# Kernel tuning notes

Measured on AMD Instinct MI355X. Metric: run time of the kernel, lower is better.

## Reference

```python
import jax, jax.numpy as jnp
import numpy as np
import math

# model dims
B, S, T = 4, 256, 8
D_MODEL, D_STATE, N_HEAD, NUM_LAYERS = 256, 128, 4, 2
VOCAB = 32000
D_HEAD = D_STATE // N_HEAD
# AdaptiveLIFNeuron constants
TAU, BASE_THR, ADAPT, TARGET = 2.0, 1.0, 0.1, 0.02
DECAY = math.exp(-1.0 / TAU)


@jax.custom_vjp
def spike_fn(x):
    # spikingjelly surrogate.ATan forward = heaviside
    return (x >= 0).astype(x.dtype)

def _spike_fwd(x):
    return spike_fn(x), x

def _spike_bwd(x, g):
    # ATan surrogate gradient, alpha=2: 1 / (1 + (pi*x)^2)
    return (g / (1.0 + (math.pi * x) ** 2),)

spike_fn.defvjp(_spike_fwd, _spike_bwd)


def lif_step(x, v, thr):
    v_pot = v * DECAY + x
    spike = spike_fn(v_pot - jax.lax.stop_gradient(thr))
    v_new = v_pot * (1.0 - jax.lax.stop_gradient(spike))  # reset where spiked
    err = jax.lax.stop_gradient(spike.mean() - TARGET)    # torch.no_grad threshold update
    thr_new = jnp.maximum(thr + ADAPT * err, 0.5)
    return spike, v_new, thr_new


def ssm_layer(x_tbsd, A, C, Wq, bq, Wkv, bkv, Wo, bo):
    # x_tbsd: [T, B, S, d_model] spikes/embeddings, scanned over time
    scale = 1.0 / math.sqrt(D_HEAD)

    def step(carry, x_t):
        h, sv, ov, ts, to = carry
        st = h @ A.T                                      # [B,S,d_state]
        q = (h @ Wq.T + bq).reshape(B * S, N_HEAD, D_HEAD)
        kv = x_t @ Wkv.T + bkv                            # [B,S,2*d_state]
        k, v = jnp.split(kv, 2, axis=-1)
        k = k.reshape(B * S, N_HEAD, D_HEAD)
        v = v.reshape(B * S, N_HEAD, D_HEAD)
        # attention across all B*S positions (faithful to torch reshape)
        scores = jnp.einsum('ahd,bhd->hab', q, k) * scale  # [H, BS, BS]
        attn = jax.nn.softmax(scores, axis=-1)
        att = jnp.einsum('hab,bhd->ahd', attn, v).reshape(B, S, D_STATE)
        upd = st + att @ Wo.T + bo
        h2, sv2, ts2 = lif_step(upd, sv, ts)
        out_pot = h2 @ C.T                                 # [B,S,d_model]
        os_, ov2, to2 = lif_step(out_pot, ov, to)
        return (h2, sv2, ov2, ts2, to2), os_

    init = (jnp.zeros((B, S, D_STATE)), jnp.zeros((B, S, D_STATE)),
            jnp.zeros((B, S, D_MODEL)),
            jnp.full((D_STATE,), BASE_THR), jnp.full((D_MODEL,), BASE_THR))
    _, outs = jax.lax.scan(step, init, x_tbsd)
    return outs  # [T,B,S,d_model]


def setup_inputs() -> dict:
    key = jax.random.key(0)
    ks = jax.random.split(key, 8)
    nrm = lambda k, shape, s: jax.random.normal(k, shape, jnp.float32) * s
    L = NUM_LAYERS
    return {
        'input_ids': jax.random.randint(ks[0], (B, S), 0, VOCAB),
        'emb': nrm(ks[1], (VOCAB, D_MODEL), 0.02),
        'A': nrm(ks[2], (L, D_STATE, D_STATE), 1.0 / math.sqrt(D_STATE)),
        'C': nrm(ks[3], (L, D_MODEL, D_STATE), 1.0 / math.sqrt(D_STATE)),
        'Wq': nrm(ks[4], (L, D_STATE, D_STATE), 1.0 / math.sqrt(D_STATE)),
        'bq': jnp.zeros((L, D_STATE)),
        'Wkv': nrm(ks[5], (L, 2 * D_STATE, D_MODEL), 1.0 / math.sqrt(D_MODEL)),
        'bkv': jnp.zeros((L, 2 * D_STATE)),
        'Wo': nrm(ks[6], (L, D_STATE, D_STATE), 1.0 / math.sqrt(D_STATE)),
        'bo': jnp.zeros((L, D_STATE)),
        'Wout': nrm(ks[7], (VOCAB, D_MODEL), 1.0 / math.sqrt(D_MODEL)),
        'bout': jnp.zeros((VOCAB,)),
    }


def reference(input_ids, emb, A, C, Wq, bq, Wkv, bkv, Wo, bo, Wout, bout):
    tok = emb[input_ids]                                   # [B,S,d_model]
    # encoder_type='expand': replicate embedding over time steps
    hidden = jnp.broadcast_to(tok[None], (T, B, S, D_MODEL))
    for l in range(NUM_LAYERS):
        hidden = ssm_layer(hidden, A[l], C[l], Wq[l], bq[l],
                           Wkv[l], bkv[l], Wo[l], bo[l])
    time_integrated = hidden.mean(axis=0)                  # mean over time -> [B,S,d_model]
    logits = time_integrated @ Wout.T + bout               # output_projection -> [B,S,vocab]
    return logits
```

## Files before the change

### kernel.cpp

```cpp
#include <hip/hip_runtime.h>
#include <math.h>

#define BS_TOT   1024
#define DM       256
#define DST      128
#define TSTEPS   8
#define DECAYF   0.6065306597126334f
#define SCALEF   0.17677669529663689f
#define NE       (BS_TOT * DM)

__global__ void embed_k(const int* __restrict__ ids, const float* __restrict__ emb,
                        float* __restrict__ tok) {
    int r = blockIdx.x, c = threadIdx.x;
    tok[r * DM + c] = emb[(size_t)ids[r] * DM + c];
}

__global__ void init_k(float* __restrict__ hb0, float* __restrict__ hb1,
                       float* __restrict__ svb0, float* __restrict__ svb1,
                       float* __restrict__ ovb0, float* __restrict__ ovb1,
                       int* __restrict__ cnts) {
    int i = blockIdx.x * 256 + threadIdx.x;
    if (i < BS_TOT * DST) { hb0[i] = 0.f; hb1[i] = 0.f; svb0[i] = 0.f; svb1[i] = 0.f; }
    ovb0[i] = 0.f; ovb1[i] = 0.f;
    if (i < 16) cnts[i] = 0;
}

__global__ __launch_bounds__(256) void ktrans_k(const float* __restrict__ kv,
                                                float* __restrict__ kT) {
    __shared__ float tile[64][133];
    const float* src = kv + (size_t)blockIdx.y * NE;
    float* dst = kT + (size_t)blockIdx.y * (128 * 1024);
    const int kc = blockIdx.x, tid = threadIdx.x;
#pragma unroll
    for (int i = 0; i < 32; ++i) {
        int idx = i * 256 + tid;
        int key = idx >> 7, d = idx & 127;
        tile[key][d] = src[(size_t)(kc * 64 + key) * 256 + d];
    }
    __syncthreads();
#pragma unroll
    for (int i = 0; i < 32; ++i) {
        int idx = i * 256 + tid;
        int d = idx >> 6, key = idx & 63;
        dst[(size_t)d * 1024 + kc * 64 + key] = tile[key][d];
    }
}

__global__ void mean_k(const float* __restrict__ outs, float* __restrict__ ti) {
    int i = blockIdx.x * 256 + threadIdx.x;
    float s = 0.f;
#pragma unroll
    for (int t = 0; t < TSTEPS; ++t) s += outs[t * NE + i];
    ti[i] = s * 0.125f;
}

template <int BM, int BN, int BK, int TM, int TN>
__global__ __launch_bounds__((BM / TM) * (BN / TN))
void gemm_k(const float* __restrict__ Amat, const float* __restrict__ Wmat,
            const float* __restrict__ bias, float* __restrict__ outp,
            int M, int N, int K) {
    constexpr int NT  = (BM / TM) * (BN / TN);
    constexpr int NXT = BN / TN;
    __shared__ float As[BK][BM + 4];
    __shared__ float Bs[BK][BN + 4];
    const int tid = threadIdx.x;
    const int n0 = blockIdx.x * BN, m0 = blockIdx.y * BM;
    const int tx = tid % NXT, ty = tid / NXT;
    float acc[TM][TN] = {};

    for (int k0 = 0; k0 < K; k0 += BK) {
#pragma unroll
        for (int i = 0; i < (BM * BK) / NT; ++i) {
            int idx = i * NT + tid;
            int kk = idx % BK, mm = idx / BK;
            As[kk][mm] = Amat[(size_t)(m0 + mm) * K + k0 + kk];
        }
#pragma unroll
        for (int i = 0; i < (BN * BK) / NT; ++i) {
            int idx = i * NT + tid;
            int kk = idx % BK, nn = idx / BK;
            Bs[kk][nn] = Wmat[(size_t)(n0 + nn) * K + k0 + kk];
        }
        __syncthreads();
#pragma unroll
        for (int kk = 0; kk < BK; ++kk) {
            float a[TM], b[TN];
#pragma unroll
            for (int i = 0; i < TM; ++i) a[i] = As[kk][ty * TM + i];
#pragma unroll
            for (int j = 0; j < TN; ++j) b[j] = Bs[kk][tx * TN + j];
#pragma unroll
            for (int i = 0; i < TM; ++i)
#pragma unroll
                for (int j = 0; j < TN; ++j) acc[i][j] += a[i] * b[j];
        }
        __syncthreads();
    }
#pragma unroll
    for (int i = 0; i < TM; ++i) {
        int mr = m0 + ty * TM + i;
#pragma unroll
        for (int j = 0; j < TN; ++j) {
            int nc = n0 + tx * TN + j;
            float x = acc[i][j];
            if (bias) x += bias[nc];
            outp[(size_t)mr * N + nc] = x;
        }
    }
}

__global__ __launch_bounds__(256) void fstep_k(
    const float* __restrict__ kT,
    const float* __restrict__ kv,
    const float* __restrict__ A_w,
    const float* __restrict__ Wq_w,
    const float* __restrict__ bq_w,
    const float* __restrict__ Wo_w,
    const float* __restrict__ bo_w,
    const float* __restrict__ C_w,
    const float* __restrict__ h_old, float* __restrict__ h_new,
    const float* __restrict__ sv_in, float* __restrict__ sv_out,
    const float* __restrict__ ov_in, float* __restrict__ ov_out,
    const float* __restrict__ att_in, float* __restrict__ att_out,
    float* __restrict__ outs_prev,
    int* __restrict__ cnt1, int* __restrict__ cnt2, int t, int do_B)
{
    __shared__ float p_s[8][1032];
    __shared__ float v_s[2][64 * 36];
    __shared__ float hA_s[8 * 128];
    __shared__ float h2_s[8 * 128];
    __shared__ float att_s[8 * 128];
    __shared__ float q_s[8 * 36];
    __shared__ float red_s[8 * 33];
    __shared__ float mrow_s[8], linv_s[8], thr_s[2];

    const int tid = threadIdx.x;
    const int hh = blockIdx.x >> 7;
    const int r0 = (blockIdx.x & 127) * 8;
    const bool wrb = (hh == 0);

    if (t > 0) {
        if (tid == 0) {
            float ts = 1.0f, to = 1.0f;
            for (int i = 0; i < t - 1; ++i) {
                float e1 = (float)cnt1[i] * (1.f / 131072.f) - 0.02f;
                ts = fmaxf(ts + 0.1f * e1, 0.5f);
                float e2 = (float)cnt2[i] * (1.f / 262144.f) - 0.02f;
                to = fmaxf(to + 0.1f * e2, 0.5f);
            }
            thr_s[0] = ts; thr_s[1] = to;
        }
#pragma unroll
        for (int i = 0; i < 4; ++i) {
            int idx = i * 256 + tid;
            hA_s[idx]  = h_old[r0 * 128 + idx];
            att_s[idx] = att_in[r0 * 128 + idx];
        }
        __syncthreads();

        {
            const int n = tid & 127, half = tid >> 7;
            const float* Ar  = A_w  + n * 128;
            const float* Wor = Wo_w + n * 128;
            float st[4] = {0.f, 0.f, 0.f, 0.f};
            float b[4]  = {0.f, 0.f, 0.f, 0.f};
            for (int k4 = 0; k4 < 32; ++k4) {
                const int k = k4 * 4;
                float4 wa = *(const float4*)(Ar + k);
                float4 wo = *(const float4*)(Wor + k);
#pragma unroll
                for (int r4 = 0; r4 < 4; ++r4) {
                    int r = half * 4 + r4;
                    float4 hv = *(const float4*)&hA_s[r * 128 + k];
                    float4 av = *(const float4*)&att_s[r * 128 + k];
                    st[r4] += hv.x * wa.x; st[r4] += hv.y * wa.y;
                    st[r4] += hv.z * wa.z; st[r4] += hv.w * wa.w;
                    b[r4] += av.x * wo.x; b[r4] += av.y * wo.y;
                    b[r4] += av.z * wo.z; b[r4] += av.w * wo.w;
                }
            }
            float ts = thr_s[0];
            int my1 = 0;
#pragma unroll
            for (int r4 = 0; r4 < 4; ++r4) {
                int r = half * 4 + r4, row = r0 + r;
                float x = b[r4] + bo_w[n];
                x += st[r4];
                float v = sv_in[row * 128 + n];
                float vp = v * DECAYF + x;
                float sp = (vp - ts >= 0.f) ? 1.f : 0.f;
                h2_s[r * 128 + n] = sp;
                if (wrb) {
                    h_new[row * 128 + n]  = sp;
                    sv_out[row * 128 + n] = vp * (1.f - sp);
                }
                my1 += (int)sp;
            }
            if (wrb) {
#pragma unroll
                for (int off = 32; off > 0; off >>= 1) my1 += __shfl_down(my1, off, 64);
                if ((tid & 63) == 0) atomicAdd(&cnt1[t - 1], my1);
            }
        }
        __syncthreads();

        if (wrb) {
            const int n = tid;
            const float* Cr = C_w + n * 128;
            float acc[8] = {0.f, 0.f, 0.f, 0.f, 0.f, 0.f, 0.f, 0.f};
            for (int k4 = 0; k4 < 32; ++k4) {
                const int k = k4 * 4;
                float4 wc = *(const float4*)(Cr + k);
#pragma unroll
                for (int r = 0; r < 8; ++r) {
                    float4 hv = *(const float4*)&h2_s[r * 128 + k];
                    acc[r] += hv.x * wc.x; acc[r] += hv.y * wc.y;
                    acc[r] += hv.z * wc.z; acc[r] += hv.w * wc.w;
                }
            }
            float to = thr_s[1];
            int my2 = 0;
#pragma unroll
            for (int r = 0; r < 8; ++r) {
                int row = r0 + r;
                float vo = ov_in[row * 256 + n];
                float vp = vo * DECAYF + acc[r];
                float sp = (vp - to >= 0.f) ? 1.f : 0.f;
                outs_prev[(size_t)row * 256 + n] = sp;
                ov_out[row * 256 + n] = vp * (1.f - sp);
                my2 += (int)sp;
            }
#pragma unroll
            for (int off = 32; off > 0; off >>= 1) my2 += __shfl_down(my2, off, 64);
            if ((tid & 63) == 0) atomicAdd(&cnt2[t - 1], my2);
        }
    } else {
#pragma unroll
        for (int i = 0; i < 4; ++i) {
            int idx = i * 256 + tid;
            h2_s[idx] = h_new[r0 * 128 + idx];
        }
        __syncthreads();
    }

    if (!do_B) return;

    {
        const int r = tid >> 5, d = tid & 31;
        const int j = hh * 32 + d;
        const float* Wqr = Wq_w + j * 128;
        float acc = 0.f;
        for (int k4 = 0; k4 < 32; ++k4) {
            const int k = k4 * 4;
            float4 wv = *(const float4*)(Wqr + k);
            float4 hv = *(const float4*)&h2_s[r * 128 + k];
            acc += hv.x * wv.x; acc += hv.y * wv.y;
            acc += hv.z * wv.z; acc += hv.w * wv.w;
        }
        q_s[r * 36 + d] = acc + bq_w[j];
    }
    __syncthreads();

    {
        const int w = tid >> 6, lane = tid & 63;
        float4 qr0[8], qr1[8];
#pragma unroll
        for (int d4 = 0; d4 < 8; ++d4) {
            qr0[d4] = *(const float4*)&q_s[(2 * w) * 36 + d4 * 4];
            qr1[d4] = *(const float4*)&q_s[(2 * w + 1) * 36 + d4 * 4];
        }
        const float* kTh = kT + hh * 32 * 1024;
        for (int kk = 0; kk < 16; ++kk) {
            const int key = kk * 64 + lane;
            float kreg[32];
#pragma unroll
            for (int d = 0; d < 32; ++d) kreg[d] = kTh[d * 1024 + key];
            float a0 = 0.f, a1 = 0.f;
#pragma unroll
            for (int d4 = 0; d4 < 8; ++d4) {
                a0 += qr0[d4].x * kreg[d4 * 4 + 0]; a0 += qr0[d4].y * kreg[d4 * 4 + 1];
                a0 += qr0[d4].z * kreg[d4 * 4 + 2]; a0 += qr0[d4].w * kreg[d4 * 4 + 3];
                a1 += qr1[d4].x * kreg[d4 * 4 + 0]; a1 += qr1[d4].y * kreg[d4 * 4 + 1];
                a1 += qr1[d4].z * kreg[d4 * 4 + 2]; a1 += qr1[d4].w * kreg[d4 * 4 + 3];
            }
            p_s[2 * w][key]     = a0 * SCALEF;
            p_s[2 * w + 1][key] = a1 * SCALEF;
        }
    }
    __syncthreads();

    {
        const int rh = tid >> 5, lg = tid & 31;
        float mx = -1e30f;
        for (int jj = 0; jj < 32; ++jj) mx = fmaxf(mx, p_s[rh][lg + 32 * jj]);
        red_s[rh * 33 + lg] = mx;
        __syncthreads();
        if (tid < 8) {
            float m = red_s[tid * 33];
            for (int j = 1; j < 32; ++j) m = fmaxf(m, red_s[tid * 33 + j]);
            mrow_s[tid] = m;
        }
        __syncthreads();
        float m = mrow_s[rh];
        float ls = 0.f;
        for (int jj = 0; jj < 32; ++jj) {
            int a = lg + 32 * jj;
            float p = expf(p_s[rh][a] - m);
            p_s[rh][a] = p;
            ls += p;
        }
        red_s[rh * 33 + lg] = ls;
        __syncthreads();
        if (tid < 8) {
            float l = 0.f;
            for (int j = 0; j < 32; ++j) l += red_s[tid * 33 + j];
            linv_s[tid] = 1.0f / l;
        }
    }
    __syncthreads();

    {
        const int rp = (tid >> 4) & 3;
        const int dp = tid & 15;
        const float4* kv4 = (const float4*)kv;
        float4 stg0, stg1;
        {
            int i0 = tid, i1 = 256 + tid;
            stg0 = kv4[(size_t)(i0 >> 3) * 64 + 32 + hh * 8 + (i0 & 7)];
            stg1 = kv4[(size_t)(i1 >> 3) * 64 + 32 + hh * 8 + (i1 & 7)];
        }
        float a00 = 0.f, a01 = 0.f, a10 = 0.f, a11 = 0.f;
        for (int c = 0; c < 16; ++c) {
            float* vb = &v_s[c & 1][0];
            {
                int i0 = tid, i1 = 256 + tid;
                *(float4*)&vb[(i0 >> 3) * 36 + (i0 & 7) * 4] = stg0;
                *(float4*)&vb[(i1 >> 3) * 36 + (i1 & 7) * 4] = stg1;
            }
            if (c < 15) {
                int i0 = tid, i1 = 256 + tid;
                stg0 = kv4[(size_t)((c + 1) * 64 + (i0 >> 3)) * 64 + 32 + hh * 8 + (i0 & 7)];
                stg1 = kv4[(size_t)((c + 1) * 64 + (i1 >> 3)) * 64 + 32 + hh * 8 + (i1 & 7)];
            }
            __syncthreads();
            if (tid < 64) {
#pragma unroll 4
                for (int k4 = 0; k4 < 16; ++k4) {
                    const int kb = k4 * 4;
                    float4 p0 = *(const float4*)&p_s[2 * rp][c * 64 + kb];
                    float4 p1 = *(const float4*)&p_s[2 * rp + 1][c * 64 + kb];
                    float2 v0 = *(const float2*)&vb[(kb + 0) * 36 + 2 * dp];
                    float2 v1 = *(const float2*)&vb[(kb + 1) * 36 + 2 * dp];
                    float2 v2 = *(const float2*)&vb[(kb + 2) * 36 + 2 * dp];
                    float2 v3 = *(const float2*)&vb[(kb + 3) * 36 + 2 * dp];
                    a00 += p0.x * v0.x; a01 += p0.x * v0.y;
                    a10 += p1.x * v0.x; a11 += p1.x * v0.y;
                    a00 += p0.y * v1.x; a01 += p0.y * v1.y;
                    a10 += p1.y * v1.x; a11 += p1.y * v1.y;
                    a00 += p0.z * v2.x; a01 += p0.z * v2.y;
                    a10 += p1.z * v2.x; a11 += p1.z * v2.y;
                    a00 += p0.w * v3.x; a01 += p0.w * v3.y;
                    a10 += p1.w * v3.x; a11 += p1.w * v3.y;
                }
            }
        }
        if (tid < 64) {
            float li0 = linv_s[2 * rp], li1 = linv_s[2 * rp + 1];
            *(float2*)&att_out[(size_t)(r0 + 2 * rp) * 128 + hh * 32 + 2 * dp] =
                make_float2(a00 * li0, a01 * li0);
            *(float2*)&att_out[(size_t)(r0 + 2 * rp + 1) * 128 + hh * 32 + 2 * dp] =
                make_float2(a10 * li1, a11 * li1);
        }
    }
}

extern "C" void kernel_launch(void* const* d_in, const int* in_sizes, int n_in,
                              void* d_out, int out_size, void* d_ws, size_t ws_size,
                              hipStream_t stream) {
    (void)in_sizes; (void)n_in; (void)out_size; (void)ws_size;
    const int*   ids  = (const int*)d_in[0];
    const float* emb  = (const float*)d_in[1];
    const float* Aw   = (const float*)d_in[2];
    const float* Cw   = (const float*)d_in[3];
    const float* Wq   = (const float*)d_in[4];
    const float* bq   = (const float*)d_in[5];
    const float* Wkv  = (const float*)d_in[6];
    const float* bkv  = (const float*)d_in[7];
    const float* Wo   = (const float*)d_in[8];
    const float* bo   = (const float*)d_in[9];
    const float* Wout = (const float*)d_in[10];
    const float* bout = (const float*)d_in[11];
    float* out = (float*)d_out;
    float* ws  = (float*)d_ws;

    float* tok  = ws;
    float* bufA = tok  + NE;
    float* bufB = bufA + 8 * NE;
    float* kvb  = bufB + 8 * NE;
    float* kTb  = kvb  + 8 * NE;
    float* attb0 = kTb  + 8 * 131072;
    float* attb1 = attb0 + 131072;
    float* hb0  = attb1 + 131072;
    float* hb1  = hb0  + 131072;
    float* svb0 = hb1  + 131072;
    float* svb1 = svb0 + 131072;
    float* ovb0 = svb1 + 131072;
    float* ovb1 = ovb0 + 262144;
    float* ti   = ovb1 + 262144;
    int*   cnts = (int*)(ti + NE);

    float* hb[2]   = {hb0, hb1};
    float* svb[2]  = {svb0, svb1};
    float* ovb[2]  = {ovb0, ovb1};
    float* attb[2] = {attb0, attb1};

    embed_k<<<dim3(1024), dim3(256), 0, stream>>>(ids, emb, tok);

    for (int l = 0; l < 2; ++l) {
        const float* Al   = Aw  + l * 16384;
        const float* Cl   = Cw  + l * 32768;
        const float* Wql  = Wq  + l * 16384;
        const float* bql  = bq  + l * 128;
        const float* Wkvl = Wkv + l * 65536;
        const float* bkvl = bkv + l * 256;
        const float* Wol  = Wo  + l * 16384;
        const float* bol  = bo  + l * 128;
        const float* xin  = (l == 0) ? tok : bufA;
        float* outs       = (l == 0) ? bufA : bufB;
        const int Mkv     = (l == 0) ? BS_TOT : 8 * BS_TOT;
        const int nt      = (l == 0) ? 1 : 8;

        init_k<<<dim3(1024), dim3(256), 0, stream>>>(hb0, hb1, svb0, svb1,
                                                     ovb0, ovb1, cnts);

        gemm_k<64, 64, 16, 4, 4><<<dim3(256 / 64, Mkv / 64), dim3(256), 0, stream>>>(
            xin, Wkvl, bkvl, kvb, Mkv, 256, 256);

        ktrans_k<<<dim3(16, nt), dim3(256), 0, stream>>>(kvb, kTb);

        for (int t = 0; t <= TSTEPS; ++t) {
            const int do_B = (t < TSTEPS) ? 1 : 0;
            const int tt = (t < TSTEPS) ? t : (TSTEPS - 1);
            const float* kT_t = (l == 0) ? kTb : kTb + (size_t)tt * 131072;
            const float* kv_t = (l == 0) ? kvb : kvb + (size_t)tt * NE;
            float* outs_prev = outs + (size_t)((t > 0) ? (t - 1) : 0) * NE;
            const int grid = do_B ? 512 : 128;
            fstep_k<<<dim3(grid), dim3(256), 0, stream>>>(
                kT_t, kv_t, Al, Wql, bql, Wol, bol, Cl,
                hb[t & 1], hb[(t + 1) & 1],
                svb[t & 1], svb[(t + 1) & 1],
                ovb[t & 1], ovb[(t + 1) & 1],
                attb[(t + 1) & 1], attb[t & 1],
                outs_prev, cnts, cnts + 8, t, do_B);
        }
    }

    mean_k<<<dim3(1024), dim3(256), 0, stream>>>(bufB, ti);

    gemm_k<64, 64, 16, 4, 4><<<dim3(32000 / 64, BS_TOT / 64), dim3(256), 0, stream>>>(
        ti, Wout, bout, out, BS_TOT, 32000, 256);
}
```

Before: 1.351 ms.

## Split fused step kernel into LIF and attention kernels with spike-sparse matvecs

```diff
diff --git a/kernel.cpp b/kernel.cpp
--- a/kernel.cpp
+++ b/kernel.cpp
@@ -15,13 +15,23 @@
     tok[r * DM + c] = emb[(size_t)ids[r] * DM + c];
 }
 
-__global__ void init_k(float* __restrict__ hb0, float* __restrict__ hb1,
-                       float* __restrict__ svb0, float* __restrict__ svb1,
-                       float* __restrict__ ovb0, float* __restrict__ ovb1,
+__global__ void prep_k(float* __restrict__ h, float* __restrict__ sv, float* __restrict__ ov,
+                       float* __restrict__ W1T, float* __restrict__ WoT, float* __restrict__ CT,
+                       const float* __restrict__ Al, const float* __restrict__ Wql,
+                       const float* __restrict__ Wol, const float* __restrict__ Cl,
                        int* __restrict__ cnts) {
     int i = blockIdx.x * 256 + threadIdx.x;
-    if (i < BS_TOT * DST) { hb0[i] = 0.f; hb1[i] = 0.f; svb0[i] = 0.f; svb1[i] = 0.f; }
-    ovb0[i] = 0.f; ovb1[i] = 0.f;
+    if (i < BS_TOT * DST) { h[i] = 0.f; sv[i] = 0.f; }
+    ov[i] = 0.f;
+    if (i < 32768) {
+        int k = i >> 8, n = i & 255;
+        W1T[i] = (n < 128) ? Al[n * 128 + k] : Wql[(n - 128) * 128 + k];
+        CT[i]  = Cl[n * 128 + k];
+    }
+    if (i < 16384) {
+        int k = i >> 7, n = i & 127;
+        WoT[i] = Wol[n * 128 + k];
+    }
     if (i < 16) cnts[i] = 0;
 }
 
@@ -109,182 +119,250 @@
     }
 }
 
-__global__ __launch_bounds__(256) void fstep_k(
+__global__ __launch_bounds__(256) void lif_k(
+    const float* __restrict__ W1T,
+    const float* __restrict__ WoT,
+    const float* __restrict__ CT,
+    const float* __restrict__ bq_w,
+    const float* __restrict__ bo_w,
+    float* __restrict__ h,
+    float* __restrict__ sv,
+    float* __restrict__ ov,
+    const float* __restrict__ att_in,
+    float* __restrict__ outs_prev,
+    float* __restrict__ q_g,
+    int* __restrict__ cnt1, int* __restrict__ cnt2, int t, int do_B)
+{
+    __shared__ float hA_s[4 * 128];
+    __shared__ float h2_s[4 * 128];
+    __shared__ float att_s[4 * 128];
+    __shared__ unsigned long long umr_s[4][2];
+    __shared__ unsigned long long um_s[2];
+    __shared__ float thr_s[2];
+
+    const int tid = threadIdx.x;
+    const int r0 = blockIdx.x * 4;
+
+    if (tid == 0) {
+        float ts = 1.0f, to = 1.0f;
+        for (int i = 0; i < t - 1; ++i) {
+            float e1 = (float)cnt1[i] * (1.f / 131072.f) - 0.02f;
+            ts = fmaxf(ts + 0.1f * e1, 0.5f);
+            float e2 = (float)cnt2[i] * (1.f / 262144.f) - 0.02f;
+            to = fmaxf(to + 0.1f * e2, 0.5f);
+        }
+        thr_s[0] = ts; thr_s[1] = to;
+    }
+    hA_s[tid]       = h[r0 * 128 + tid];
+    hA_s[256 + tid] = h[r0 * 128 + 256 + tid];
+    if (t > 0) {
+        att_s[tid]       = att_in[r0 * 128 + tid];
+        att_s[256 + tid] = att_in[r0 * 128 + 256 + tid];
+    }
+    __syncthreads();
+    {
+        int w = tid >> 6, l = tid & 63;
+        unsigned long long b0 = __ballot(hA_s[w * 128 + l] != 0.f);
+        unsigned long long b1 = __ballot(hA_s[w * 128 + 64 + l] != 0.f);
+        if (l == 0) { umr_s[w][0] = b0; umr_s[w][1] = b1; }
+    }
+    __syncthreads();
+    if (tid == 0) {
+        um_s[0] = umr_s[0][0] | umr_s[1][0] | umr_s[2][0] | umr_s[3][0];
+        um_s[1] = umr_s[0][1] | umr_s[1][1] | umr_s[2][1] | umr_s[3][1];
+    }
+    __syncthreads();
+
+    const int n = tid & 127, half = tid >> 7;
+    const int ra = half * 2, rb = half * 2 + 1;
+
+    if (t > 0) {
+        float sta = 0.f, stb = 0.f;
+        unsigned long long u = um_s[0];
+        while (u) {
+            int k = __builtin_ctzll(u); u &= u - 1;
+            float w = W1T[(k << 8) + n];
+            sta += hA_s[ra * 128 + k] * w; stb += hA_s[rb * 128 + k] * w;
+        }
+        u = um_s[1];
+        while (u) {
+            int kk = __builtin_ctzll(u); u &= u - 1;
+            int k = 64 + kk;
+            float w = W1T[(k << 8) + n];
+            sta += hA_s[ra * 128 + k] * w; stb += hA_s[rb * 128 + k] * w;
+        }
+        float ba = 0.f, bb = 0.f;
+        for (int i4 = 0; i4 < 32; ++i4) {
+            const int i = i4 * 4;
+            float w0 = WoT[(i + 0) * 128 + n];
+            float w1 = WoT[(i + 1) * 128 + n];
+            float w2 = WoT[(i + 2) * 128 + n];
+            float w3 = WoT[(i + 3) * 128 + n];
+            float4 aa = *(const float4*)&att_s[ra * 128 + i];
+            float4 ab = *(const float4*)&att_s[rb * 128 + i];
+            ba += aa.x * w0; ba += aa.y * w1; ba += aa.z * w2; ba += aa.w * w3;
+            bb += ab.x * w0; bb += ab.y * w1; bb += ab.z * w2; bb += ab.w * w3;
+        }
+        float ts = thr_s[0];
+        float xa = ba + bo_w[n]; xa += sta;
+        float va = sv[(r0 + ra) * 128 + n];
+        float vpa = va * DECAYF + xa;
+        float spa = (vpa - ts >= 0.f) ? 1.f : 0.f;
+        h[(r0 + ra) * 128 + n]  = spa;
+        sv[(r0 + ra) * 128 + n] = vpa * (1.f - spa);
+        h2_s[ra * 128 + n] = spa;
+
+        float xb = bb + bo_w[n]; xb += stb;
+        float vb = sv[(r0 + rb) * 128 + n];
+        float vpb = vb * DECAYF + xb;
+        float spb = (vpb - ts >= 0.f) ? 1.f : 0.f;
+        h[(r0 + rb) * 128 + n]  = spb;
+        sv[(r0 + rb) * 128 + n] = vpb * (1.f - spb);
+        h2_s[rb * 128 + n] = spb;
+
+        unsigned long long bba = __ballot(spa != 0.f);
+        unsigned long long bbb = __ballot(spb != 0.f);
+        int w = tid >> 6, l = tid & 63;
+        if (l == 0) {
+            umr_s[ra][w & 1] = bba;
+            umr_s[rb][w & 1] = bbb;
+            atomicAdd(&cnt1[t - 1], __popcll(bba) + __popcll(bbb));
+        }
+    } else {
+        h2_s[tid]       = hA_s[tid];
+        h2_s[256 + tid] = hA_s[256 + tid];
+    }
+    __syncthreads();
+    if (tid == 0) {
+        um_s[0] = umr_s[0][0] | umr_s[1][0] | umr_s[2][0] | umr_s[3][0];
+        um_s[1] = umr_s[0][1] | umr_s[1][1] | umr_s[2][1] | umr_s[3][1];
+    }
+    __syncthreads();
+
+    if (t > 0) {
+        const int n2 = tid;
+        float a0 = 0.f, a1 = 0.f, a2 = 0.f, a3 = 0.f;
+        unsigned long long u = um_s[0];
+        while (u) {
+            int k = __builtin_ctzll(u); u &= u - 1;
+            float w = CT[(k << 8) + n2];
+            a0 += h2_s[k] * w;       a1 += h2_s[128 + k] * w;
+            a2 += h2_s[256 + k] * w; a3 += h2_s[384 + k] * w;
+        }
+        u = um_s[1];
+        while (u) {
+            int kk = __builtin_ctzll(u); u &= u - 1;
+            int k = 64 + kk;
+            float w = CT[(k << 8) + n2];
+            a0 += h2_s[k] * w;       a1 += h2_s[128 + k] * w;
+            a2 += h2_s[256 + k] * w; a3 += h2_s[384 + k] * w;
+        }
+        float to = thr_s[1];
+        float accs[4] = {a0, a1, a2, a3};
+        float sp[4];
+#pragma unroll
+        for (int r = 0; r < 4; ++r) {
+            float vo = ov[(r0 + r) * 256 + n2];
+            float vp = vo * DECAYF + accs[r];
+            float s = (vp - to >= 0.f) ? 1.f : 0.f;
+            sp[r] = s;
+            outs_prev[(size_t)(r0 + r) * 256 + n2] = s;
+            ov[(r0 + r) * 256 + n2] = vp * (1.f - s);
+        }
+        unsigned long long c0 = __ballot(sp[0] != 0.f);
+        unsigned long long c1 = __ballot(sp[1] != 0.f);
+        unsigned long long c2 = __ballot(sp[2] != 0.f);
+        unsigned long long c3 = __ballot(sp[3] != 0.f);
+        if ((tid & 63) == 0)
+            atomicAdd(&cnt2[t - 1], __popcll(c0) + __popcll(c1) + __popcll(c2) + __popcll(c3));
+    }
+
+    if (do_B) {
+        float qa = 0.f, qb = 0.f;
+        unsigned long long u = um_s[0];
+        while (u) {
+            int k = __builtin_ctzll(u); u &= u - 1;
+            float w = W1T[(k << 8) + 128 + n];
+            qa += h2_s[ra * 128 + k] * w; qb += h2_s[rb * 128 + k] * w;
+        }
+        u = um_s[1];
+        while (u) {
+            int kk = __builtin_ctzll(u); u &= u - 1;
+            int k = 64 + kk;
+            float w = W1T[(k << 8) + 128 + n];
+            qa += h2_s[ra * 128 + k] * w; qb += h2_s[rb * 128 + k] * w;
+        }
+        q_g[(r0 + ra) * 128 + n] = qa + bq_w[n];
+        q_g[(r0 + rb) * 128 + n] = qb + bq_w[n];
+    }
+}
+
+__global__ __launch_bounds__(256) void attn_k(
+    const float* __restrict__ q_g,
     const float* __restrict__ kT,
     const float* __restrict__ kv,
-    const float* __restrict__ A_w,
-    const float* __restrict__ Wq_w,
-    const float* __restrict__ bq_w,
-    const float* __restrict__ Wo_w,
-    const float* __restrict__ bo_w,
-    const float* __restrict__ C_w,
-    const float* __restrict__ h_old, float* __restrict__ h_new,
-    const float* __restrict__ sv_in, float* __restrict__ sv_out,
-    const float* __restrict__ ov_in, float* __restrict__ ov_out,
-    const float* __restrict__ att_in, float* __restrict__ att_out,
-    float* __restrict__ outs_prev,
-    int* __restrict__ cnt1, int* __restrict__ cnt2, int t, int do_B)
+    float* __restrict__ att_out)
 {
     __shared__ float p_s[8][1032];
-    __shared__ float v_s[2][64 * 36];
-    __shared__ float hA_s[8 * 128];
-    __shared__ float h2_s[8 * 128];
-    __shared__ float att_s[8 * 128];
-    __shared__ float q_s[8 * 36];
+    __shared__ float v_s[64 * 36];
+    __shared__ float q_s[8][32];
     __shared__ float red_s[8 * 33];
-    __shared__ float mrow_s[8], linv_s[8], thr_s[2];
+    __shared__ float mrow_s[8], linv_s[8];
 
     const int tid = threadIdx.x;
     const int hh = blockIdx.x >> 7;
     const int r0 = (blockIdx.x & 127) * 8;
-    const bool wrb = (hh == 0);
-
-    if (t > 0) {
-        if (tid == 0) {
-            float ts = 1.0f, to = 1.0f;
-            for (int i = 0; i < t - 1; ++i) {
-                float e1 = (float)cnt1[i] * (1.f / 131072.f) - 0.02f;
-                ts = fmaxf(ts + 0.1f * e1, 0.5f);
-                float e2 = (float)cnt2[i] * (1.f / 262144.f) - 0.02f;
-                to = fmaxf(to + 0.1f * e2, 0.5f);
-            }
-            thr_s[0] = ts; thr_s[1] = to;
-        }
-#pragma unroll
-        for (int i = 0; i < 4; ++i) {
-            int idx = i * 256 + tid;
-            hA_s[idx]  = h_old[r0 * 128 + idx];
-            att_s[idx] = att_in[r0 * 128 + idx];
-        }
-        __syncthreads();
-
-        {
-            const int n = tid & 127, half = tid >> 7;
-            const float* Ar  = A_w  + n * 128;
-            const float* Wor = Wo_w + n * 128;
-            float st[4] = {0.f, 0.f, 0.f, 0.f};
-            float b[4]  = {0.f, 0.f, 0.f, 0.f};
-            for (int k4 = 0; k4 < 32; ++k4) {
-                const int k = k4 * 4;
-                float4 wa = *(const float4*)(Ar + k);
-                float4 wo = *(const float4*)(Wor + k);
-#pragma unroll
-                for (int r4 = 0; r4 < 4; ++r4) {
-                    int r = half * 4 + r4;
-                    float4 hv = *(const float4*)&hA_s[r * 128 + k];
-                    float4 av = *(const float4*)&att_s[r * 128 + k];
-                    st[r4] += hv.x * wa.x; st[r4] += hv.y * wa.y;
-                    st[r4] += hv.z * wa.z; st[r4] += hv.w * wa.w;
-                    b[r4] += av.x * wo.x; b[r4] += av.y * wo.y;
-                    b[r4] += av.z * wo.z; b[r4] += av.w * wo.w;
+
+    {
+        int r = tid >> 5, d = tid & 31;
+        q_s[r][d] = q_g[(size_t)(r0 + r) * 128 + hh * 32 + d];
+    }
+    __syncthreads();
+
+    {
+        const int w = tid >> 6, l = tid & 63;
+        const int key4 = w * 64 + l;
+        const float4* kT4 = (const float4*)(kT + (size_t)hh * 32 * 1024);
+        float4 acc[8];
+#pragma unroll
+        for (int pass = 0; pass < 2; ++pass) {
+            const int d0 = pass * 16;
+            float4 kreg[16];
+#pragma unroll
+            for (int i = 0; i < 16; ++i) kreg[i] = kT4[(size_t)(d0 + i) * 256 + key4];
+#pragma unroll
+            for (int r = 0; r < 8; ++r)
+                acc[r] = pass ? *(const float4*)&p_s[r][key4 * 4]
+                              : make_float4(0.f, 0.f, 0.f, 0.f);
+#pragma unroll
+            for (int i4 = 0; i4 < 4; ++i4) {
+#pragma unroll
+                for (int r = 0; r < 8; ++r) {
+                    float4 qv = *(const float4*)&q_s[r][d0 + i4 * 4];
+                    float4 k0 = kreg[i4 * 4 + 0], k1 = kreg[i4 * 4 + 1];
+                    float4 k2 = kreg[i4 * 4 + 2], k3 = kreg[i4 * 4 + 3];
+                    acc[r].x += qv.x * k0.x; acc[r].x += qv.y * k1.x;
+                    acc[r].x += qv.z * k2.x; acc[r].x += qv.w * k3.x;
+                    acc[r].y += qv.x * k0.y; acc[r].y += qv.y * k1.y;
+                    acc[r].y += qv.z * k2.y; acc[r].y += qv.w * k3.y;
+                    acc[r].z += qv.x * k0.z; acc[r].z += qv.y * k1.z;
+                    acc[r].z += qv.z * k2.z; acc[r].z += qv.w * k3.z;
+                    acc[r].w += qv.x * k0.w; acc[r].w += qv.y * k1.w;
+                    acc[r].w += qv.z * k2.w; acc[r].w += qv.w * k3.w;
                 }
             }
-            float ts = thr_s[0];
-            int my1 = 0;
-#pragma unroll
-            for (int r4 = 0; r4 < 4; ++r4) {
-                int r = half * 4 + r4, row = r0 + r;
-                float x = b[r4] + bo_w[n];
-                x += st[r4];
-                float v = sv_in[row * 128 + n];
-                float vp = v * DECAYF + x;
-                float sp = (vp - ts >= 0.f) ? 1.f : 0.f;
-                h2_s[r * 128 + n] = sp;
-                if (wrb) {
-                    h_new[row * 128 + n]  = sp;
-                    sv_out[row * 128 + n] = vp * (1.f - sp);
-                }
-                my1 += (int)sp;
-            }
-            if (wrb) {
-#pragma unroll
-                for (int off = 32; off > 0; off >>= 1) my1 += __shfl_down(my1, off, 64);
-                if ((tid & 63) == 0) atomicAdd(&cnt1[t - 1], my1);
-            }
-        }
-        __syncthreads();
-
-        if (wrb) {
-            const int n = tid;
-            const float* Cr = C_w + n * 128;
-            float acc[8] = {0.f, 0.f, 0.f, 0.f, 0.f, 0.f, 0.f, 0.f};
-            for (int k4 = 0; k4 < 32; ++k4) {
-                const int k = k4 * 4;
-                float4 wc = *(const float4*)(Cr + k);
+            if (pass == 0) {
+#pragma unroll
+                for (int r = 0; r < 8; ++r)
+                    *(float4*)&p_s[r][key4 * 4] = acc[r];
+            } else {
 #pragma unroll
                 for (int r = 0; r < 8; ++r) {
-                    float4 hv = *(const float4*)&h2_s[r * 128 + k];
-                    acc[r] += hv.x * wc.x; acc[r] += hv.y * wc.y;
-                    acc[r] += hv.z * wc.z; acc[r] += hv.w * wc.w;
+                    acc[r].x *= SCALEF; acc[r].y *= SCALEF;
+                    acc[r].z *= SCALEF; acc[r].w *= SCALEF;
+                    *(float4*)&p_s[r][key4 * 4] = acc[r];
                 }
             }
-            float to = thr_s[1];
-            int my2 = 0;
-#pragma unroll
-            for (int r = 0; r < 8; ++r) {
-                int row = r0 + r;
-                float vo = ov_in[row * 256 + n];
-                float vp = vo * DECAYF + acc[r];
-                float sp = (vp - to >= 0.f) ? 1.f : 0.f;
-                outs_prev[(size_t)row * 256 + n] = sp;
-                ov_out[row * 256 + n] = vp * (1.f - sp);
-                my2 += (int)sp;
-            }
-#pragma unroll
-            for (int off = 32; off > 0; off >>= 1) my2 += __shfl_down(my2, off, 64);
-            if ((tid & 63) == 0) atomicAdd(&cnt2[t - 1], my2);
-        }
-    } else {
-#pragma unroll
-        for (int i = 0; i < 4; ++i) {
-            int idx = i * 256 + tid;
-            h2_s[idx] = h_new[r0 * 128 + idx];
-        }
-        __syncthreads();
-    }
-
-    if (!do_B) return;
-
-    {
-        const int r = tid >> 5, d = tid & 31;
-        const int j = hh * 32 + d;
-        const float* Wqr = Wq_w + j * 128;
-        float acc = 0.f;
-        for (int k4 = 0; k4 < 32; ++k4) {
-            const int k = k4 * 4;
-            float4 wv = *(const float4*)(Wqr + k);
-            float4 hv = *(const float4*)&h2_s[r * 128 + k];
-            acc += hv.x * wv.x; acc += hv.y * wv.y;
-            acc += hv.z * wv.z; acc += hv.w * wv.w;
-        }
-        q_s[r * 36 + d] = acc + bq_w[j];
-    }
-    __syncthreads();
-
-    {
-        const int w = tid >> 6, lane = tid & 63;
-        float4 qr0[8], qr1[8];
-#pragma unroll
-        for (int d4 = 0; d4 < 8; ++d4) {
-            qr0[d4] = *(const float4*)&q_s[(2 * w) * 36 + d4 * 4];
-            qr1[d4] = *(const float4*)&q_s[(2 * w + 1) * 36 + d4 * 4];
-        }
-        const float* kTh = kT + hh * 32 * 1024;
-        for (int kk = 0; kk < 16; ++kk) {
-            const int key = kk * 64 + lane;
-            float kreg[32];
-#pragma unroll
-            for (int d = 0; d < 32; ++d) kreg[d] = kTh[d * 1024 + key];
-            float a0 = 0.f, a1 = 0.f;
-#pragma unroll
-            for (int d4 = 0; d4 < 8; ++d4) {
-                a0 += qr0[d4].x * kreg[d4 * 4 + 0]; a0 += qr0[d4].y * kreg[d4 * 4 + 1];
-                a0 += qr0[d4].z * kreg[d4 * 4 + 2]; a0 += qr0[d4].w * kreg[d4 * 4 + 3];
-                a1 += qr1[d4].x * kreg[d4 * 4 + 0]; a1 += qr1[d4].y * kreg[d4 * 4 + 1];
-                a1 += qr1[d4].z * kreg[d4 * 4 + 2]; a1 += qr1[d4].w * kreg[d4 * 4 + 3];
-            }
-            p_s[2 * w][key]     = a0 * SCALEF;
-            p_s[2 * w + 1][key] = a1 * SCALEF;
         }
     }
     __syncthreads();
@@ -320,8 +398,10 @@
     __syncthreads();
 
     {
-        const int rp = (tid >> 4) & 3;
-        const int dp = tid & 15;
+        const int w = tid >> 6, l = tid & 63;
+        const int r = (w & 1) * 4 + (l >> 4);
+        const int dp = l & 15;
+        const bool act = (w < 2);
         const float4* kv4 = (const float4*)kv;
         float4 stg0, stg1;
         {
@@ -329,13 +409,12 @@
             stg0 = kv4[(size_t)(i0 >> 3) * 64 + 32 + hh * 8 + (i0 & 7)];
             stg1 = kv4[(size_t)(i1 >> 3) * 64 + 32 + hh * 8 + (i1 & 7)];
         }
-        float a00 = 0.f, a01 = 0.f, a10 = 0.f, a11 = 0.f;
+        float a0 = 0.f, a1 = 0.f;
         for (int c = 0; c < 16; ++c) {
-            float* vb = &v_s[c & 1][0];
             {
                 int i0 = tid, i1 = 256 + tid;
-                *(float4*)&vb[(i0 >> 3) * 36 + (i0 & 7) * 4] = stg0;
-                *(float4*)&vb[(i1 >> 3) * 36 + (i1 & 7) * 4] = stg1;
+                *(float4*)&v_s[(i0 >> 3) * 36 + (i0 & 7) * 4] = stg0;
+                *(float4*)&v_s[(i1 >> 3) * 36 + (i1 & 7) * 4] = stg1;
             }
             if (c < 15) {
                 int i0 = tid, i1 = 256 + tid;
@@ -343,33 +422,27 @@
                 stg1 = kv4[(size_t)((c + 1) * 64 + (i1 >> 3)) * 64 + 32 + hh * 8 + (i1 & 7)];
             }
             __syncthreads();
-            if (tid < 64) {
+            if (act) {
 #pragma unroll 4
                 for (int k4 = 0; k4 < 16; ++k4) {
                     const int kb = k4 * 4;
-                    float4 p0 = *(const float4*)&p_s[2 * rp][c * 64 + kb];
-                    float4 p1 = *(const float4*)&p_s[2 * rp + 1][c * 64 + kb];
-                    float2 v0 = *(const float2*)&vb[(kb + 0) * 36 + 2 * dp];
-                    float2 v1 = *(const float2*)&vb[(kb + 1) * 36 + 2 * dp];
-                    float2 v2 = *(const float2*)&vb[(kb + 2) * 36 + 2 * dp];
-                    float2 v3 = *(const float2*)&vb[(kb + 3) * 36 + 2 * dp];
-                    a00 += p0.x * v0.x; a01 += p0.x * v0.y;
-                    a10 += p1.x * v0.x; a11 += p1.x * v0.y;
-                    a00 += p0.y * v1.x; a01 += p0.y * v1.y;
-                    a10 += p1.y * v1.x; a11 += p1.y * v1.y;
-                    a00 += p0.z * v2.x; a01 += p0.z * v2.y;
-                    a10 += p1.z * v2.x; a11 += p1.z * v2.y;
-                    a00 += p0.w * v3.x; a01 += p0.w * v3.y;
-                    a10 += p1.w * v3.x; a11 += p1.w * v3.y;
+                    float4 p4 = *(const float4*)&p_s[r][c * 64 + kb];
+                    float2 v0 = *(const float2*)&v_s[(kb + 0) * 36 + 2 * dp];
+                    float2 v1 = *(const float2*)&v_s[(kb + 1) * 36 + 2 * dp];
+                    float2 v2 = *(const float2*)&v_s[(kb + 2) * 36 + 2 * dp];
+                    float2 v3 = *(const float2*)&v_s[(kb + 3) * 36 + 2 * dp];
+                    a0 += p4.x * v0.x; a1 += p4.x * v0.y;
+                    a0 += p4.y * v1.x; a1 += p4.y * v1.y;
+                    a0 += p4.z * v2.x; a1 += p4.z * v2.y;
+                    a0 += p4.w * v3.x; a1 += p4.w * v3.y;
                 }
             }
-        }
-        if (tid < 64) {
-            float li0 = linv_s[2 * rp], li1 = linv_s[2 * rp + 1];
-            *(float2*)&att_out[(size_t)(r0 + 2 * rp) * 128 + hh * 32 + 2 * dp] =
-                make_float2(a00 * li0, a01 * li0);
-            *(float2*)&att_out[(size_t)(r0 + 2 * rp + 1) * 128 + hh * 32 + 2 * dp] =
-                make_float2(a10 * li1, a11 * li1);
+            __syncthreads();
+        }
+        if (act) {
+            float li = linv_s[r];
+            *(float2*)&att_out[(size_t)(r0 + r) * 128 + hh * 32 + 2 * dp] =
+                make_float2(a0 * li, a1 * li);
         }
     }
 }
@@ -398,21 +471,16 @@
     float* bufB = bufA + 8 * NE;
     float* kvb  = bufB + 8 * NE;
     float* kTb  = kvb  + 8 * NE;
-    float* attb0 = kTb  + 8 * 131072;
-    float* attb1 = attb0 + 131072;
-    float* hb0  = attb1 + 131072;
-    float* hb1  = hb0  + 131072;
-    float* svb0 = hb1  + 131072;
-    float* svb1 = svb0 + 131072;
-    float* ovb0 = svb1 + 131072;
-    float* ovb1 = ovb0 + 262144;
-    float* ti   = ovb1 + 262144;
-    int*   cnts = (int*)(ti + NE);
-
-    float* hb[2]   = {hb0, hb1};
-    float* svb[2]  = {svb0, svb1};
-    float* ovb[2]  = {ovb0, ovb1};
-    float* attb[2] = {attb0, attb1};
+    float* attb = kTb  + 8 * 131072;
+    float* hbuf = attb + 131072;
+    float* svb  = hbuf + 131072;
+    float* ovb  = svb  + 131072;
+    float* qg   = ovb  + 262144;
+    float* ti   = qg   + 131072;
+    float* W1T  = ti   + NE;
+    float* WoT  = W1T  + 32768;
+    float* CT   = WoT  + 16384;
+    int*   cnts = (int*)(CT + 32768);
 
     embed_k<<<dim3(1024), dim3(256), 0, stream>>>(ids, emb, tok);
 
@@ -430,8 +498,8 @@
         const int Mkv     = (l == 0) ? BS_TOT : 8 * BS_TOT;
         const int nt      = (l == 0) ? 1 : 8;
 
-        init_k<<<dim3(1024), dim3(256), 0, stream>>>(hb0, hb1, svb0, svb1,
-                                                     ovb0, ovb1, cnts);
+        prep_k<<<dim3(1024), dim3(256), 0, stream>>>(hbuf, svb, ovb, W1T, WoT, CT,
+                                                     Al, Wql, Wol, Cl, cnts);
 
         gemm_k<64, 64, 16, 4, 4><<<dim3(256 / 64, Mkv / 64), dim3(256), 0, stream>>>(
             xin, Wkvl, bkvl, kvb, Mkv, 256, 256);
@@ -440,18 +508,16 @@
 
         for (int t = 0; t <= TSTEPS; ++t) {
             const int do_B = (t < TSTEPS) ? 1 : 0;
-            const int tt = (t < TSTEPS) ? t : (TSTEPS - 1);
-            const float* kT_t = (l == 0) ? kTb : kTb + (size_t)tt * 131072;
-            const float* kv_t = (l == 0) ? kvb : kvb + (size_t)tt * NE;
             float* outs_prev = outs + (size_t)((t > 0) ? (t - 1) : 0) * NE;
-            const int grid = do_B ? 512 : 128;
-            fstep_k<<<dim3(grid), dim3(256), 0, stream>>>(
-                kT_t, kv_t, Al, Wql, bql, Wol, bol, Cl,
-                hb[t & 1], hb[(t + 1) & 1],
-                svb[t & 1], svb[(t + 1) & 1],
-                ovb[t & 1], ovb[(t + 1) & 1],
-                attb[(t + 1) & 1], attb[t & 1],
-                outs_prev, cnts, cnts + 8, t, do_B);
+            lif_k<<<dim3(256), dim3(256), 0, stream>>>(
+                W1T, WoT, CT, bql, bol,
+                hbuf, svb, ovb, attb, outs_prev, qg,
+                cnts, cnts + 8, t, do_B);
+            if (do_B) {
+                const float* kT_t = (l == 0) ? kTb : kTb + (size_t)t * 131072;
+                const float* kv_t = (l == 0) ? kvb : kvb + (size_t)t * NE;
+                attn_k<<<dim3(512), dim3(256), 0, stream>>>(qg, kT_t, kv_t, attb);
+            }
         }
     }
 
```

Measured after the change: 1.247 ms. 1.08x faster.
